# Performance work log

Measured on AMD Instinct MI355X. Metric: run time of the kernel, lower is better.

The kernel has to match this reference:

```python
import jax, jax.numpy as jnp
import numpy as np

N_NODES = 100000


def gcn_layer(x, W, b, src, dst, n):
    # PyG GCNConv: h = x @ W, then D^{-1/2}(A+I)D^{-1/2} aggregation, then + b
    h = x @ W  # [N, out]
    ones = jnp.ones(src.shape[0], dtype=h.dtype)
    deg = jax.ops.segment_sum(ones, dst, num_segments=n) + 1.0  # +1 for self loop
    dinv = jax.lax.rsqrt(deg)  # [N]
    norm = dinv[src] * dinv[dst]  # [E]
    msgs = h[src] * norm[:, None]  # gather + scale, [E, out]
    agg = jax.ops.segment_sum(msgs, dst, num_segments=n)
    agg = agg + h * (dinv * dinv)[:, None]  # self-loop term
    return agg + b


def setup_inputs() -> dict:
    key = jax.random.key(0)
    k1, k2, k3, k4, k5, k6 = jax.random.split(key, 6)
    in_dim, h1, h2 = 256, 128, 64
    x = jax.random.normal(k1, (N_NODES, in_dim), dtype=jnp.float32)
    edge_index = jax.random.randint(k2, (2, 1600000), 0, N_NODES, dtype=jnp.int64)
    # Glorot-style init for weights, zeros for bias (PyG default)
    W1 = jax.random.normal(k3, (in_dim, h1), dtype=jnp.float32) / np.sqrt(in_dim)
    b1 = jnp.zeros((h1,), dtype=jnp.float32)
    W2 = jax.random.normal(k4, (h1, h2), dtype=jnp.float32) / np.sqrt(h1)
    b2 = jnp.zeros((h2,), dtype=jnp.float32)
    return {"x": x, "W1": W1, "b1": b1, "W2": W2, "b2": b2, "edge_index": edge_index}


def reference(x, W1, b1, W2, b2, edge_index):
    src, dst = edge_index[0], edge_index[1]
    n = x.shape[0]
    h = jax.nn.relu(gcn_layer(x, W1, b1, src, dst, n))
    h = jax.nn.relu(gcn_layer(h, W2, b2, src, dst, n))
    return h
```

## Files before the change

kernel.cpp:

```cpp
#include <hip/hip_runtime.h>
#include <hip/hip_bf16.h>


typedef __attribute__((ext_vector_type(8))) short bf16x8;
typedef __attribute__((ext_vector_type(4))) float f32x4;

__device__ inline unsigned short f2bf(float f) {
    unsigned u = __float_as_uint(f);
    u = (u + 0x7fff + ((u >> 16) & 1)) >> 16;
    return (unsigned short)u;
}
__device__ inline float bf2f(unsigned short h) {
    return __uint_as_float(((unsigned)h) << 16);
}
__device__ inline float bflo(unsigned u) { return __uint_as_float(u << 16); }
__device__ inline float bfhi(unsigned u) { return __uint_as_float(u & 0xffff0000u); }

__global__ void hist_kernel(const int* __restrict__ dst, int* __restrict__ deg, int E) {
    int stride = gridDim.x * blockDim.x;
    for (int i = blockIdx.x * blockDim.x + threadIdx.x; i < E; i += stride)
        atomicAdd(&deg[dst[i]], 1);
}

__global__ __launch_bounds__(1024) void scan_partial_kernel(const int* __restrict__ deg,
        int* __restrict__ psum, float* __restrict__ dinv, int n) {
    __shared__ int wsum[16];
    int tid = threadIdx.x, wave = tid >> 6, lane = tid & 63;
    int i0 = blockIdx.x * 4096 + tid * 4;
    int v0 = 0, v1 = 0, v2 = 0, v3 = 0;
    if (i0 + 3 < n) {
        int4 v = *(const int4*)(deg + i0);
        v0 = v.x; v1 = v.y; v2 = v.z; v3 = v.w;
    } else {
        if (i0 + 0 < n) v0 = deg[i0 + 0];
        if (i0 + 1 < n) v1 = deg[i0 + 1];
        if (i0 + 2 < n) v2 = deg[i0 + 2];
        if (i0 + 3 < n) v3 = deg[i0 + 3];
    }
    if (i0 + 0 < n) dinv[i0 + 0] = 1.0f / sqrtf((float)v0 + 1.0f);
    if (i0 + 1 < n) dinv[i0 + 1] = 1.0f / sqrtf((float)v1 + 1.0f);
    if (i0 + 2 < n) dinv[i0 + 2] = 1.0f / sqrtf((float)v2 + 1.0f);
    if (i0 + 3 < n) dinv[i0 + 3] = 1.0f / sqrtf((float)v3 + 1.0f);
    int s = v0 + v1 + v2 + v3;
    #pragma unroll
    for (int off = 1; off < 64; off <<= 1) s += __shfl_xor(s, off, 64);
    if (lane == 0) wsum[wave] = s;
    __syncthreads();
    if (tid == 0) {
        int t = 0;
        #pragma unroll
        for (int w = 0; w < 16; ++w) t += wsum[w];
        psum[blockIdx.x] = t;
    }
}

__global__ void scan_base_kernel(int* __restrict__ psum, int* __restrict__ offs,
                                 int nb, int n) {
    int lane = threadIdx.x;
    int v = (lane < nb) ? psum[lane] : 0;
    int x = v;
    #pragma unroll
    for (int off = 1; off < 64; off <<= 1) {
        int y = __shfl_up(x, off, 64);
        if (lane >= off) x += y;
    }
    if (lane < nb) psum[lane] = x - v;
    if (lane == 63) offs[n] = x;
}

__global__ __launch_bounds__(1024) void scan_local_kernel(const int* __restrict__ deg,
        const int* __restrict__ psum, int* __restrict__ offs, int n) {
    __shared__ int wsum[16];
    int tid = threadIdx.x, wave = tid >> 6, lane = tid & 63;
    int i0 = blockIdx.x * 4096 + tid * 4;
    int v0 = 0, v1 = 0, v2 = 0, v3 = 0;
    if (i0 + 3 < n) {
        int4 v = *(const int4*)(deg + i0);
        v0 = v.x; v1 = v.y; v2 = v.z; v3 = v.w;
    } else {
        if (i0 + 0 < n) v0 = deg[i0 + 0];
        if (i0 + 1 < n) v1 = deg[i0 + 1];
        if (i0 + 2 < n) v2 = deg[i0 + 2];
        if (i0 + 3 < n) v3 = deg[i0 + 3];
    }
    int s = v0 + v1 + v2 + v3;
    int x = s;
    #pragma unroll
    for (int off = 1; off < 64; off <<= 1) {
        int y = __shfl_up(x, off, 64);
        if (lane >= off) x += y;
    }
    if (lane == 63) wsum[wave] = x;
    __syncthreads();
    int wbase = 0;
    #pragma unroll
    for (int w = 0; w < 16; ++w)
        if (w < wave) wbase += wsum[w];
    int ex = psum[blockIdx.x] + wbase + (x - s);
    if (i0 + 0 < n) offs[i0 + 0] = ex;
    if (i0 + 1 < n) offs[i0 + 1] = ex + v0;
    if (i0 + 2 < n) offs[i0 + 2] = ex + v0 + v1;
    if (i0 + 3 < n) offs[i0 + 3] = ex + v0 + v1 + v2;
}

__global__ void fill_kernel(const int* __restrict__ src, const int* __restrict__ dst,
        const int* __restrict__ offs, int* __restrict__ cursor,
        int* __restrict__ csr, int E) {
    int stride = gridDim.x * blockDim.x;
    for (int i = blockIdx.x * blockDim.x + threadIdx.x; i < E; i += stride) {
        int d = dst[i];
        int pos = offs[d] + atomicAdd(&cursor[d], 1);
        csr[pos] = src[i];
    }
}

__global__ void wsplit_kernel(const float* __restrict__ W,
        unsigned short* __restrict__ Wt_hi, unsigned short* __restrict__ Wt_lo,
        int K, int N) {
    int idx = blockIdx.x * 256 + threadIdx.x;
    if (idx >= K * N) return;
    int k = idx / N, n = idx - k * N;
    float v = W[idx];
    unsigned short h = f2bf(v);
    unsigned short l = f2bf(v - bf2f(h));
    Wt_hi[(size_t)n * K + k] = h;
    Wt_lo[(size_t)n * K + k] = l;
}

template <int K, int NT>
__global__ __launch_bounds__(256) void gemm_mfma_kernel(const float* __restrict__ X,
        const unsigned short* __restrict__ Wt_hi, const unsigned short* __restrict__ Wt_lo,
        const float* __restrict__ dinv, unsigned short* __restrict__ G, int M) {
    constexpr int N   = NT * 16;
    constexpr int BK  = 32;
    constexpr int LDA = BK + 8;
    __shared__ unsigned short Ah[128 * LDA];
    __shared__ unsigned short Al[128 * LDA];

    const int tid  = threadIdx.x;
    const int wv   = tid >> 6, ln = tid & 63;
    const int l16  = ln & 15, kseg = ln >> 4;
    const int brow = blockIdx.x * 128;

    f32x4 acc[2][NT];
    #pragma unroll
    for (int a = 0; a < 2; ++a)
        #pragma unroll
        for (int b = 0; b < NT; ++b) acc[a][b] = 0;

    const int srow = tid >> 1;
    const int scol = (tid & 1) * 16;
    int grow = brow + srow;
    if (grow >= M) grow = M - 1;
    const float* xrow = X + (size_t)grow * K + scol;
    unsigned int* ahw = (unsigned int*)&Ah[srow * LDA + scol];
    unsigned int* alw = (unsigned int*)&Al[srow * LDA + scol];

    const int arow = wv * 32;

    for (int k0 = 0; k0 < K; k0 += BK) {
        float4 q0 = *(const float4*)(xrow + k0 + 0);
        float4 q1 = *(const float4*)(xrow + k0 + 4);
        float4 q2 = *(const float4*)(xrow + k0 + 8);
        float4 q3 = *(const float4*)(xrow + k0 + 12);
        float v[16] = {q0.x,q0.y,q0.z,q0.w, q1.x,q1.y,q1.z,q1.w,
                       q2.x,q2.y,q2.z,q2.w, q3.x,q3.y,q3.z,q3.w};
        unsigned hw[8], lw[8];
        #pragma unroll
        for (int j = 0; j < 8; ++j) {
            unsigned short h0 = f2bf(v[2*j]),   h1 = f2bf(v[2*j+1]);
            unsigned short l0 = f2bf(v[2*j]   - bf2f(h0));
            unsigned short l1 = f2bf(v[2*j+1] - bf2f(h1));
            hw[j] = (unsigned)h0 | ((unsigned)h1 << 16);
            lw[j] = (unsigned)l0 | ((unsigned)l1 << 16);
        }
        *(uint4*)(ahw + 0) = make_uint4(hw[0], hw[1], hw[2], hw[3]);
        *(uint4*)(ahw + 4) = make_uint4(hw[4], hw[5], hw[6], hw[7]);
        *(uint4*)(alw + 0) = make_uint4(lw[0], lw[1], lw[2], lw[3]);
        *(uint4*)(alw + 4) = make_uint4(lw[4], lw[5], lw[6], lw[7]);
        __syncthreads();

        bf16x8 a_h[2], a_l[2];
        #pragma unroll
        for (int tr = 0; tr < 2; ++tr) {
            a_h[tr] = *(const bf16x8*)&Ah[(arow + tr * 16 + l16) * LDA + kseg * 8];
            a_l[tr] = *(const bf16x8*)&Al[(arow + tr * 16 + l16) * LDA + kseg * 8];
        }
        #pragma unroll
        for (int tc = 0; tc < NT; ++tc) {
            size_t wo = (size_t)(tc * 16 + l16) * K + k0 + kseg * 8;
            bf16x8 b_h = *(const bf16x8*)(Wt_hi + wo);
            bf16x8 b_l = *(const bf16x8*)(Wt_lo + wo);
            #pragma unroll
            for (int tr = 0; tr < 2; ++tr) {
                acc[tr][tc] = __builtin_amdgcn_mfma_f32_16x16x32_bf16(a_h[tr], b_h, acc[tr][tc], 0, 0, 0);
                acc[tr][tc] = __builtin_amdgcn_mfma_f32_16x16x32_bf16(a_l[tr], b_h, acc[tr][tc], 0, 0, 0);
                acc[tr][tc] = __builtin_amdgcn_mfma_f32_16x16x32_bf16(a_h[tr], b_l, acc[tr][tc], 0, 0, 0);
            }
        }
        __syncthreads();
    }

    #pragma unroll
    for (int tr = 0; tr < 2; ++tr) {
        int rbase = brow + arow + tr * 16 + (ln >> 4) * 4;
        #pragma unroll
        for (int r = 0; r < 4; ++r) {
            int row = rbase + r;
            if (row < M) {
                float dv = dinv[row];
                #pragma unroll
                for (int tc = 0; tc < NT; ++tc)
                    G[(size_t)row * N + tc * 16 + l16] = f2bf(acc[tr][tc][r] * dv);
            }
        }
    }
}

__global__ __launch_bounds__(256) void aggregate128_kernel(const unsigned* __restrict__ G,
        const int* __restrict__ csr, const int* __restrict__ offs,
        const float* __restrict__ dinv, const float* __restrict__ bias,
        float* __restrict__ out, int n) {
    int wave = threadIdx.x >> 6, lane = threadIdx.x & 63;
    int node = blockIdx.x * 4 + wave;
    if (node >= n) return;
    int beg = offs[node], end = offs[node + 1];

    unsigned u = G[(size_t)node * 64 + lane];
    float a0 = bflo(u), a1 = bfhi(u);
    int e = beg;
    for (; e + 4 <= end; e += 4) {
        int s0 = csr[e], s1 = csr[e + 1], s2 = csr[e + 2], s3 = csr[e + 3];
        unsigned u0 = G[(size_t)s0 * 64 + lane];
        unsigned u1 = G[(size_t)s1 * 64 + lane];
        unsigned u2 = G[(size_t)s2 * 64 + lane];
        unsigned u3 = G[(size_t)s3 * 64 + lane];
        a0 += (bflo(u0) + bflo(u1)) + (bflo(u2) + bflo(u3));
        a1 += (bfhi(u0) + bfhi(u1)) + (bfhi(u2) + bfhi(u3));
    }
    for (; e < end; ++e) {
        unsigned u0 = G[(size_t)csr[e] * 64 + lane];
        a0 += bflo(u0);
        a1 += bfhi(u0);
    }
    float di = dinv[node];
    float2 r;
    r.x = fmaxf(fmaf(a0, di, bias[lane * 2 + 0]), 0.0f);
    r.y = fmaxf(fmaf(a1, di, bias[lane * 2 + 1]), 0.0f);
    ((float2*)(out + (size_t)node * 128))[lane] = r;
}

__global__ __launch_bounds__(256) void aggregate64_kernel(const unsigned* __restrict__ G,
        const int* __restrict__ csr, const int* __restrict__ offs,
        const float* __restrict__ dinv, const float* __restrict__ bias,
        float* __restrict__ out, int n) {
    int wave = threadIdx.x >> 6, lane = threadIdx.x & 63;
    int node = blockIdx.x * 4 + wave;
    if (node >= n) return;
    int beg = offs[node], end = offs[node + 1];
    int half = lane >> 5, col = lane & 31;

    float a0 = 0.0f, a1 = 0.0f;
    if (half == 0) {
        unsigned u = G[(size_t)node * 32 + col];
        a0 = bflo(u); a1 = bfhi(u);
    }
    int e = beg;
    for (; e + 4 <= end; e += 4) {
        int sA = csr[e + half], sB = csr[e + 2 + half];
        unsigned uA = G[(size_t)sA * 32 + col];
        unsigned uB = G[(size_t)sB * 32 + col];
        a0 += bflo(uA) + bflo(uB);
        a1 += bfhi(uA) + bfhi(uB);
    }
    if (e + 2 <= end) {
        int sA = csr[e + half];
        unsigned uA = G[(size_t)sA * 32 + col];
        a0 += bflo(uA);
        a1 += bfhi(uA);
        e += 2;
    }
    if (e < end && half == 0) {
        unsigned uA = G[(size_t)csr[e] * 32 + col];
        a0 += bflo(uA);
        a1 += bfhi(uA);
    }
    a0 += __shfl_down(a0, 32, 64);
    a1 += __shfl_down(a1, 32, 64);
    if (half == 0) {
        float di = dinv[node];
        float2 r;
        r.x = fmaxf(fmaf(a0, di, bias[col * 2 + 0]), 0.0f);
        r.y = fmaxf(fmaf(a1, di, bias[col * 2 + 1]), 0.0f);
        ((float2*)(out + (size_t)node * 64))[col] = r;
    }
}

extern "C" void kernel_launch(void* const* d_in, const int* in_sizes, int n_in,
                              void* d_out, int out_size, void* d_ws, size_t ws_size,
                              hipStream_t stream) {
    const float* x  = (const float*)d_in[0];
    const float* W1 = (const float*)d_in[1];
    const float* b1 = (const float*)d_in[2];
    const float* W2 = (const float*)d_in[3];
    const float* b2 = (const float*)d_in[4];
    const int* edge = (const int*)d_in[5];

    const int IN = 256, H1 = 128, H2 = 64;
    const int E = in_sizes[5] / 2;
    const int N = in_sizes[0] / IN;
    const int* srcp = edge;
    const int* dstp = edge + E;

    char* ws = (char*)d_ws;
    auto alignup = [](size_t v) { return (v + 255) & ~(size_t)255; };
    size_t off = 0;
    size_t degSz = alignup((size_t)N * 4);
    int*            deg    = (int*)(ws + off);            off += degSz;
    int*            cursor = (int*)(ws + off);            off += degSz;
    int*            offs   = (int*)(ws + off);            off += alignup(((size_t)N + 1) * 4);
    float*          dinv   = (float*)(ws + off);          off += degSz;
    int*            psum   = (int*)(ws + off);            off += alignup(64 * 4);
    int*            csr    = (int*)(ws + off);            off += alignup((size_t)E * 4);
    unsigned short* wt1h   = (unsigned short*)(ws + off); off += alignup((size_t)IN * H1 * 2);
    unsigned short* wt1l   = (unsigned short*)(ws + off); off += alignup((size_t)IN * H1 * 2);
    unsigned short* wt2h   = (unsigned short*)(ws + off); off += alignup((size_t)H1 * H2 * 2);
    unsigned short* wt2l   = (unsigned short*)(ws + off); off += alignup((size_t)H1 * H2 * 2);
    unsigned short* g1     = (unsigned short*)(ws + off); off += alignup((size_t)N * H1 * 2);
    float*          h1     = (float*)(ws + off);          off += alignup((size_t)N * H1 * 4);
    unsigned short* g2     = g1;

    hipMemsetAsync(deg, 0, 2 * degSz, stream);

    int egrid = (E + 255) / 256;
    if (egrid > 2048) egrid = 2048;
    int sb = (N + 4095) / 4096;

    hist_kernel<<<egrid, 256, 0, stream>>>(dstp, deg, E);
    scan_partial_kernel<<<sb, 1024, 0, stream>>>(deg, psum, dinv, N);
    scan_base_kernel<<<1, 64, 0, stream>>>(psum, offs, sb, N);
    scan_local_kernel<<<sb, 1024, 0, stream>>>(deg, psum, offs, N);
    fill_kernel<<<egrid, 256, 0, stream>>>(srcp, dstp, offs, cursor, csr, E);
    wsplit_kernel<<<(IN * H1 + 255) / 256, 256, 0, stream>>>(W1, wt1h, wt1l, IN, H1);
    wsplit_kernel<<<(H1 * H2 + 255) / 256, 256, 0, stream>>>(W2, wt2h, wt2l, H1, H2);

    int mgrid = (N + 127) / 128;
    int agrid = (N + 3) / 4;

    gemm_mfma_kernel<256, 8><<<mgrid, 256, 0, stream>>>(x, wt1h, wt1l, dinv, g1, N);
    aggregate128_kernel<<<agrid, 256, 0, stream>>>((const unsigned*)g1, csr, offs,
                                                   dinv, b1, h1, N);
    gemm_mfma_kernel<128, 4><<<mgrid, 256, 0, stream>>>(h1, wt2h, wt2l, dinv, g2, N);
    aggregate64_kernel<<<agrid, 256, 0, stream>>>((const unsigned*)g2, csr, offs,
                                                  dinv, b2, (float*)d_out, N);
}
```

Measured before the change: 558.9 us.

## Shrink GEMM row tile to 64, split waves across columns, prefetch next X slice

The MFMA GEMM block tile drops from 128 rows to 64 rows, doubling the number of blocks. For the first layer the four waves are arranged as a 2x2 grid over rows and columns instead of stacking all four along rows. The next K-slice of X is also loaded into registers before the current slice's MFMA work, so global latency overlaps compute. The aim is more parallelism and latency hiding in exchange for more redundant W reads per output row.

```diff
diff --git a/kernel.cpp b/kernel.cpp
--- a/kernel.cpp
+++ b/kernel.cpp
@@ -127,72 +127,75 @@
     Wt_lo[(size_t)n * K + k] = l;
 }
 
-template <int K, int NT>
+template <int K, int N, int NWC>
 __global__ __launch_bounds__(256) void gemm_mfma_kernel(const float* __restrict__ X,
         const unsigned short* __restrict__ Wt_hi, const unsigned short* __restrict__ Wt_lo,
         const float* __restrict__ dinv, unsigned short* __restrict__ G, int M) {
-    constexpr int N   = NT * 16;
     constexpr int BK  = 32;
+    constexpr int BM  = 64;
     constexpr int LDA = BK + 8;
-    __shared__ unsigned short Ah[128 * LDA];
-    __shared__ unsigned short Al[128 * LDA];
+    constexpr int RW  = NWC;
+    constexpr int CW  = N / 16 / NWC;
+    __shared__ unsigned short Ah[BM * LDA];
+    __shared__ unsigned short Al[BM * LDA];
 
     const int tid  = threadIdx.x;
     const int wv   = tid >> 6, ln = tid & 63;
     const int l16  = ln & 15, kseg = ln >> 4;
-    const int brow = blockIdx.x * 128;
-
-    f32x4 acc[2][NT];
-    #pragma unroll
-    for (int a = 0; a < 2; ++a)
-        #pragma unroll
-        for (int b = 0; b < NT; ++b) acc[a][b] = 0;
-
-    const int srow = tid >> 1;
-    const int scol = (tid & 1) * 16;
+    const int wc   = wv % NWC, wr = wv / NWC;
+    const int brow = blockIdx.x * BM;
+
+    f32x4 acc[RW][CW];
+    #pragma unroll
+    for (int a = 0; a < RW; ++a)
+        #pragma unroll
+        for (int b = 0; b < CW; ++b) acc[a][b] = 0;
+
+    const int srow = tid >> 2;
+    const int scol = (tid & 3) * 8;
     int grow = brow + srow;
     if (grow >= M) grow = M - 1;
-    const float* xrow = X + (size_t)grow * K + scol;
+    const float* xp = X + (size_t)grow * K + scol;
     unsigned int* ahw = (unsigned int*)&Ah[srow * LDA + scol];
     unsigned int* alw = (unsigned int*)&Al[srow * LDA + scol];
 
-    const int arow = wv * 32;
+    float4 qa = *(const float4*)(xp);
+    float4 qb = *(const float4*)(xp + 4);
 
     for (int k0 = 0; k0 < K; k0 += BK) {
-        float4 q0 = *(const float4*)(xrow + k0 + 0);
-        float4 q1 = *(const float4*)(xrow + k0 + 4);
-        float4 q2 = *(const float4*)(xrow + k0 + 8);
-        float4 q3 = *(const float4*)(xrow + k0 + 12);
-        float v[16] = {q0.x,q0.y,q0.z,q0.w, q1.x,q1.y,q1.z,q1.w,
-                       q2.x,q2.y,q2.z,q2.w, q3.x,q3.y,q3.z,q3.w};
-        unsigned hw[8], lw[8];
-        #pragma unroll
-        for (int j = 0; j < 8; ++j) {
+        float v[8] = {qa.x, qa.y, qa.z, qa.w, qb.x, qb.y, qb.z, qb.w};
+        unsigned hw[4], lw[4];
+        #pragma unroll
+        for (int j = 0; j < 4; ++j) {
             unsigned short h0 = f2bf(v[2*j]),   h1 = f2bf(v[2*j+1]);
             unsigned short l0 = f2bf(v[2*j]   - bf2f(h0));
             unsigned short l1 = f2bf(v[2*j+1] - bf2f(h1));
             hw[j] = (unsigned)h0 | ((unsigned)h1 << 16);
             lw[j] = (unsigned)l0 | ((unsigned)l1 << 16);
         }
-        *(uint4*)(ahw + 0) = make_uint4(hw[0], hw[1], hw[2], hw[3]);
-        *(uint4*)(ahw + 4) = make_uint4(hw[4], hw[5], hw[6], hw[7]);
-        *(uint4*)(alw + 0) = make_uint4(lw[0], lw[1], lw[2], lw[3]);
-        *(uint4*)(alw + 4) = make_uint4(lw[4], lw[5], lw[6], lw[7]);
+        *(uint4*)ahw = make_uint4(hw[0], hw[1], hw[2], hw[3]);
+        *(uint4*)alw = make_uint4(lw[0], lw[1], lw[2], lw[3]);
         __syncthreads();
 
-        bf16x8 a_h[2], a_l[2];
-        #pragma unroll
-        for (int tr = 0; tr < 2; ++tr) {
-            a_h[tr] = *(const bf16x8*)&Ah[(arow + tr * 16 + l16) * LDA + kseg * 8];
-            a_l[tr] = *(const bf16x8*)&Al[(arow + tr * 16 + l16) * LDA + kseg * 8];
-        }
-        #pragma unroll
-        for (int tc = 0; tc < NT; ++tc) {
-            size_t wo = (size_t)(tc * 16 + l16) * K + k0 + kseg * 8;
+        if (k0 + BK < K) {
+            qa = *(const float4*)(xp + k0 + BK);
+            qb = *(const float4*)(xp + k0 + BK + 4);
+        }
+
+        bf16x8 a_h[RW], a_l[RW];
+        #pragma unroll
+        for (int tr = 0; tr < RW; ++tr) {
+            int ar = wr * (RW * 16) + tr * 16 + l16;
+            a_h[tr] = *(const bf16x8*)&Ah[ar * LDA + kseg * 8];
+            a_l[tr] = *(const bf16x8*)&Al[ar * LDA + kseg * 8];
+        }
+        #pragma unroll
+        for (int tc = 0; tc < CW; ++tc) {
+            size_t wo = (size_t)(wc * (CW * 16) + tc * 16 + l16) * K + k0 + kseg * 8;
             bf16x8 b_h = *(const bf16x8*)(Wt_hi + wo);
             bf16x8 b_l = *(const bf16x8*)(Wt_lo + wo);
             #pragma unroll
-            for (int tr = 0; tr < 2; ++tr) {
+            for (int tr = 0; tr < RW; ++tr) {
                 acc[tr][tc] = __builtin_amdgcn_mfma_f32_16x16x32_bf16(a_h[tr], b_h, acc[tr][tc], 0, 0, 0);
                 acc[tr][tc] = __builtin_amdgcn_mfma_f32_16x16x32_bf16(a_l[tr], b_h, acc[tr][tc], 0, 0, 0);
                 acc[tr][tc] = __builtin_amdgcn_mfma_f32_16x16x32_bf16(a_h[tr], b_l, acc[tr][tc], 0, 0, 0);
@@ -202,16 +205,17 @@
     }
 
     #pragma unroll
-    for (int tr = 0; tr < 2; ++tr) {
-        int rbase = brow + arow + tr * 16 + (ln >> 4) * 4;
+    for (int tr = 0; tr < RW; ++tr) {
+        int rbase = brow + wr * (RW * 16) + tr * 16 + (ln >> 4) * 4;
         #pragma unroll
         for (int r = 0; r < 4; ++r) {
             int row = rbase + r;
             if (row < M) {
                 float dv = dinv[row];
                 #pragma unroll
-                for (int tc = 0; tc < NT; ++tc)
-                    G[(size_t)row * N + tc * 16 + l16] = f2bf(acc[tr][tc][r] * dv);
+                for (int tc = 0; tc < CW; ++tc)
+                    G[(size_t)row * N + wc * (CW * 16) + tc * 16 + l16] =
+                        f2bf(acc[tr][tc][r] * dv);
             }
         }
     }
@@ -344,13 +348,13 @@
     wsplit_kernel<<<(IN * H1 + 255) / 256, 256, 0, stream>>>(W1, wt1h, wt1l, IN, H1);
     wsplit_kernel<<<(H1 * H2 + 255) / 256, 256, 0, stream>>>(W2, wt2h, wt2l, H1, H2);
 
-    int mgrid = (N + 127) / 128;
+    int mgrid = (N + 63) / 64;
     int agrid = (N + 3) / 4;
 
-    gemm_mfma_kernel<256, 8><<<mgrid, 256, 0, stream>>>(x, wt1h, wt1l, dinv, g1, N);
+    gemm_mfma_kernel<256, 128, 2><<<mgrid, 256, 0, stream>>>(x, wt1h, wt1l, dinv, g1, N);
     aggregate128_kernel<<<agrid, 256, 0, stream>>>((const unsigned*)g1, csr, offs,
                                                    dinv, b1, h1, N);
-    gemm_mfma_kernel<128, 4><<<mgrid, 256, 0, stream>>>(h1, wt2h, wt2l, dinv, g2, N);
+    gemm_mfma_kernel<128, 64, 1><<<mgrid, 256, 0, stream>>>(h1, wt2h, wt2l, dinv, g2, N);
     aggregate64_kernel<<<agrid, 256, 0, stream>>>((const unsigned*)g2, csr, offs,
                                                   dinv, b2, (float*)d_out, N);
 }
```

Result: faster. 538.9 us (-3.6%).
